# Kernel tuning notes

Hardware: AMD Instinct MI355X
Metric: run time of the kernel (lower is better)

The kernel has to match this reference:

```python
import jax, jax.numpy as jnp
import numpy as np

BITS = 3
LEVELS = 2 ** BITS            # 8
HALF_RANGE = (LEVELS - 1) / 2  # 3.5
INCREMENT = 1.0 / (LEVELS // 2)  # 0.25


def setup_inputs() -> dict:
    key = jax.random.key(0)
    kq, kk, kv, kr = jax.random.split(key, 4)
    B, H, S, D = 2, 16, 2048, 128
    q = jax.random.normal(kq, (B, H, S, D), dtype=jnp.float32)
    k = jax.random.normal(kk, (B, H, S, D), dtype=jnp.float32)
    v = jax.random.normal(kv, (B, H, S, D), dtype=jnp.float32)
    # random orthogonal rotation (QR of a Gaussian), as in PolarQuant.__init__
    Hmat = jax.random.normal(kr, (D, D), dtype=jnp.float32)
    R, _ = jnp.linalg.qr(Hmat)
    qjl_scale = jnp.full((1,), 0.01, dtype=jnp.float32)
    return {"q": q, "k": k, "v": v, "R": R, "qjl_scale": qjl_scale}


def _compress_decompress(x, R, qjl_scale):
    """PolarQuant rotate -> QJL 3-bit quantize (+ sign correction) -> dequantize -> inverse rotate."""
    B, Hh, S, D = x.shape
    xr = jnp.einsum('bhsd,de->bhse', x, R)            # rotate: x @ R
    x_max = jnp.abs(xr).max() + 1e-8                   # global scale (as in quantize/compress)
    xs = xr / x_max * HALF_RANGE                       # scale to [-3.5, 3.5]
    xq = jnp.clip(jnp.round(xs / INCREMENT) * INCREMENT, -HALF_RANGE, HALF_RANGE)
    residual = xs - xq
    xc = xq + jnp.sign(residual) * qjl_scale[0] * x_max  # QJL 1-bit correction
    xd = xc / HALF_RANGE * x_max                       # dequantize
    xo = jnp.einsum('bhse,de->bhsd', xd, R)            # inverse rotate: y @ R.T
    return xo


def reference(q, k, v, R, qjl_scale):
    D = q.shape[-1]
    k_approx = _compress_decompress(k, R, qjl_scale)
    v_approx = _compress_decompress(v, R, qjl_scale)
    scores = jnp.einsum('bhqd,bhkd->bhqk', q, k_approx) / jnp.sqrt(jnp.float32(D))
    attn = jax.nn.softmax(scores, axis=-1)
    out = jnp.einsum('bhqk,bhkd->bhqd', attn, v_approx)
    return out
```

## Files before the change

kernel.cpp:

```cpp
#include <hip/hip_runtime.h>


typedef float    f32x4  __attribute__((ext_vector_type(4)));
typedef float    f32x16 __attribute__((ext_vector_type(16)));
typedef __bf16   bf16x8 __attribute__((ext_vector_type(8)));
typedef __bf16   bf16x4 __attribute__((ext_vector_type(4)));
typedef _Float16 f16x8  __attribute__((ext_vector_type(8)));
typedef unsigned long long u64;

#define SLEN 2048
#define DH   128

static __device__ __forceinline__ f32x16 zero16() {
  f32x16 z;
#pragma unroll
  for (int i = 0; i < 16; ++i) z[i] = 0.f;
  return z;
}

static __device__ __forceinline__ f32x16 mfma_bf16_32x32x16(bf16x8 a, bf16x8 b, f32x16 c) {
  return __builtin_amdgcn_mfma_f32_32x32x16_bf16(a, b, c, 0, 0, 0);
}
static __device__ __forceinline__ f32x16 mfma_f16_32x32x16(f16x8 a, f16x8 b, f32x16 c) {
  return __builtin_amdgcn_mfma_f32_32x32x16_f16(a, b, c, 0, 0, 0);
}

static __device__ __forceinline__ void lds_dma16(const void* g, void* l) {
  __builtin_amdgcn_global_load_lds(
      (const __attribute__((address_space(1))) void*)(unsigned long long)g,
      (__attribute__((address_space(3))) void*)(unsigned int)(unsigned long long)l,
      16, 0, 0);
}

static __device__ __forceinline__ float qdq(float xr, float xmax, float qs) {
  float xs = xr / xmax * 3.5f;
  float xq = rintf(xs * 4.0f) * 0.25f;
  xq = fminf(3.5f, fmaxf(-3.5f, xq));
  float res = xs - xq;
  float sg = (res > 0.0f) ? 1.0f : ((res < 0.0f) ? -1.0f : 0.0f);
  float xc = xq + sg * qs * xmax;
  return xc / 3.5f * xmax;
}

static __device__ __forceinline__ unsigned short bfbits(float f) {
  __bf16 b = (__bf16)f;
  return __builtin_bit_cast(unsigned short, b);
}

__global__ __launch_bounds__(256) void prep_R(
    const float* __restrict__ R, _Float16* __restrict__ Bhi,
    _Float16* __restrict__ Blo, _Float16* __restrict__ BhiT,
    _Float16* __restrict__ BloT)
{
  int i = blockIdx.x * 256 + threadIdx.x;
  int kk = i >> 7, n = i & 127;
  float r = R[i];
  _Float16 h = (_Float16)r;
  _Float16 l = (_Float16)(r - (float)h);
  Bhi[i] = h; Blo[i] = l;
  BhiT[n * 128 + kk] = h; BloT[n * 128 + kk] = l;
}

__global__ __launch_bounds__(256) void rot_all_kernel(
    const float* __restrict__ K, const float* __restrict__ V,
    const float* __restrict__ Q, const _Float16* __restrict__ Gh,
    const _Float16* __restrict__ Gl, float* __restrict__ kr,
    float* __restrict__ vr, float* __restrict__ kpart,
    float* __restrict__ vpart, __bf16* __restrict__ qb,
    float* __restrict__ qn)
{
  __shared__ _Float16 BH[128 * 128];

  const int tid = threadIdx.x, wave = tid >> 6, lane = tid & 63;
  const int r31 = lane & 31, hi = lane >> 5;
  const int bid = blockIdx.x;

  int stage_n[8], stage_ch[8], stage_dst[8];
#pragma unroll
  for (int u = 0; u < 8; ++u) {
    int c = (wave * 8 + u) * 64 + lane;
    stage_n[u] = c >> 4;
    stage_ch[u] = (c & 15) ^ (stage_n[u] & 7);
    stage_dst[u] = (wave * 8 + u) * 512;
  }

  if (bid < 1024) {
    const bool isv = bid >= 512;
    const int b = bid & 511;
    const float* X = isv ? V : K;
    float* OUT = isv ? vr : kr;
    float* part = isv ? vpart : kpart;
    const long r0 = (long)b * 128;

#pragma unroll
    for (int u = 0; u < 8; ++u)
      lds_dma16(Gh + stage_n[u] * 128 + stage_ch[u] * 8, BH + stage_dst[u]);

    const long rowg = r0 + wave * 32 + r31;
    f16x8 ah[8], al[8];
#pragma unroll
    for (int t = 0; t < 8; ++t) {
      f32x4 x0 = *(const f32x4*)&X[rowg * 128 + t * 16 + hi * 8];
      f32x4 x1 = *(const f32x4*)&X[rowg * 128 + t * 16 + hi * 8 + 4];
#pragma unroll
      for (int j = 0; j < 4; ++j) {
        _Float16 h0 = (_Float16)x0[j]; ah[t][j] = h0;
        _Float16 h1 = (_Float16)x1[j]; ah[t][4 + j] = h1;
        al[t][j]     = (_Float16)(x0[j] - (float)h0);
        al[t][4 + j] = (_Float16)(x1[j] - (float)h1);
      }
    }
    __syncthreads();

    f32x16 acc[4];
#pragma unroll
    for (int ct = 0; ct < 4; ++ct) acc[ct] = zero16();
#pragma unroll
    for (int ct = 0; ct < 4; ++ct) {
#pragma unroll
      for (int t = 0; t < 8; ++t) {
        int idx = (ct * 32 + r31) * 128 + (((2 * t + hi) ^ (r31 & 7)) * 8);
        f16x8 bh = *(const f16x8*)&BH[idx];
        acc[ct] = mfma_f16_32x32x16(ah[t], bh, acc[ct]);
        acc[ct] = mfma_f16_32x32x16(al[t], bh, acc[ct]);
      }
    }

    __syncthreads();
#pragma unroll
    for (int u = 0; u < 8; ++u)
      lds_dma16(Gl + stage_n[u] * 128 + stage_ch[u] * 8, BH + stage_dst[u]);
    __syncthreads();

#pragma unroll
    for (int ct = 0; ct < 4; ++ct) {
#pragma unroll
      for (int t = 0; t < 8; ++t) {
        int idx = (ct * 32 + r31) * 128 + (((2 * t + hi) ^ (r31 & 7)) * 8);
        f16x8 bl = *(const f16x8*)&BH[idx];
        acc[ct] = mfma_f16_32x32x16(ah[t], bl, acc[ct]);
      }
    }

    float am = 0.f;
#pragma unroll
    for (int ct = 0; ct < 4; ++ct)
#pragma unroll
      for (int r = 0; r < 16; ++r) {
        long grow = r0 + wave * 32 + (r & 3) + 8 * (r >> 2) + 4 * hi;
        float v = acc[ct][r];
        OUT[grow * 128 + ct * 32 + r31] = v;
        am = fmaxf(am, fabsf(v));
      }
#pragma unroll
    for (int m = 1; m <= 32; m <<= 1) am = fmaxf(am, __shfl_xor(am, m, 64));
    if (lane == 0) part[b * 4 + wave] = am;

  } else {
    const int b = bid - 1024;
    const long r0 = (long)b * 128;

#pragma unroll
    for (int u = 0; u < 8; ++u)
      lds_dma16(Gh + stage_n[u] * 128 + stage_ch[u] * 8, BH + stage_dst[u]);

    const long rowg = r0 + wave * 32 + r31;
    f16x8 ah[8];
#pragma unroll
    for (int t = 0; t < 8; ++t) {
      f32x4 x0 = *(const f32x4*)&Q[rowg * 128 + t * 16 + hi * 8];
      f32x4 x1 = *(const f32x4*)&Q[rowg * 128 + t * 16 + hi * 8 + 4];
#pragma unroll
      for (int j = 0; j < 4; ++j) {
        ah[t][j]     = (_Float16)x0[j];
        ah[t][4 + j] = (_Float16)x1[j];
      }
    }
    __syncthreads();

    f32x16 acc[4];
#pragma unroll
    for (int ct = 0; ct < 4; ++ct) acc[ct] = zero16();
#pragma unroll
    for (int ct = 0; ct < 4; ++ct) {
#pragma unroll
      for (int t = 0; t < 8; ++t) {
        int idx = (ct * 32 + r31) * 128 + (((2 * t + hi) ^ (r31 & 7)) * 8);
        f16x8 bh = *(const f16x8*)&BH[idx];
        acc[ct] = mfma_f16_32x32x16(ah[t], bh, acc[ct]);
      }
    }

    const float sc = 0.12751743342f;
    float rs[16];
#pragma unroll
    for (int r = 0; r < 16; ++r) rs[r] = 0.f;
#pragma unroll
    for (int ct = 0; ct < 4; ++ct)
#pragma unroll
      for (int r = 0; r < 16; ++r) {
        long grow = r0 + wave * 32 + (r & 3) + 8 * (r >> 2) + 4 * hi;
        __bf16 bb = (__bf16)(acc[ct][r] * sc);
        qb[grow * 128 + ct * 32 + r31] = bb;
        float fb = (float)bb;
        rs[r] += fb * fb;
      }
#pragma unroll
    for (int r = 0; r < 16; ++r) {
#pragma unroll
      for (int msk = 1; msk <= 16; msk <<= 1) rs[r] += __shfl_xor(rs[r], msk, 64);
      if (r31 == r)
        qn[r0 + wave * 32 + (r & 3) + 8 * (r >> 2) + 4 * hi] = sqrtf(rs[r]);
    }
  }
}

__global__ __launch_bounds__(256) void rot_o_kernel(
    const _Float16* __restrict__ X, const _Float16* __restrict__ Gh,
    float* __restrict__ OUT)
{
  __shared__ _Float16 BH[128 * 128];

  const int tid = threadIdx.x, wave = tid >> 6, lane = tid & 63;
  const int r31 = lane & 31, hi = lane >> 5;
  const long r0 = (long)blockIdx.x * 128;

#pragma unroll
  for (int u = 0; u < 8; ++u) {
    int c = (wave * 8 + u) * 64 + lane;
    int n = c >> 4, p = c & 15, ch = p ^ (n & 7);
    lds_dma16(Gh + n * 128 + ch * 8, BH + (wave * 8 + u) * 512);
  }

  const long rowg = r0 + wave * 32 + r31;
  f16x8 ah[8];
#pragma unroll
  for (int t = 0; t < 8; ++t)
    ah[t] = *(const f16x8*)&X[rowg * 128 + t * 16 + hi * 8];
  __syncthreads();

  f32x16 acc[4];
#pragma unroll
  for (int ct = 0; ct < 4; ++ct) acc[ct] = zero16();
#pragma unroll
  for (int ct = 0; ct < 4; ++ct) {
#pragma unroll
    for (int t = 0; t < 8; ++t) {
      int idx = (ct * 32 + r31) * 128 + (((2 * t + hi) ^ (r31 & 7)) * 8);
      f16x8 bh = *(const f16x8*)&BH[idx];
      acc[ct] = mfma_f16_32x32x16(ah[t], bh, acc[ct]);
    }
  }
#pragma unroll
  for (int ct = 0; ct < 4; ++ct)
#pragma unroll
    for (int r = 0; r < 16; ++r) {
      long grow = r0 + wave * 32 + (r & 3) + 8 * (r >> 2) + 4 * hi;
      OUT[grow * 128 + ct * 32 + r31] = acc[ct][r];
    }
}

__global__ __launch_bounds__(256) void quantize_vt_kernel(
    const float* __restrict__ vr, const float* __restrict__ vpart,
    const float* __restrict__ qjl, u64* __restrict__ vdt2)
{
  __shared__ unsigned int Ts32[128][18];
  __shared__ float sm[4];
  const int tid = threadIdx.x;

  float m = 0.f;
  for (int i = tid; i < 2048; i += 256) m = fmaxf(m, vpart[i]);
#pragma unroll
  for (int msk = 1; msk <= 32; msk <<= 1) m = fmaxf(m, __shfl_xor(m, msk, 64));
  if ((tid & 63) == 0) sm[tid >> 6] = m;
  __syncthreads();
  const float xmax = fmaxf(fmaxf(sm[0], sm[1]), fmaxf(sm[2], sm[3])) + 1e-8f;
  const float qs = qjl[0];

  const int bh = blockIdx.x >> 6, blk = blockIdx.x & 63;
  const int s0 = blk * 32;
  const int sp  = tid & 15;
  const int dch = tid >> 4;
  const long rb = (long)bh * SLEN + s0;
  const float* p0 = &vr[(rb + sp * 2    ) * 128 + dch * 8];
  const float* p1 = &vr[(rb + sp * 2 + 1) * 128 + dch * 8];
#pragma unroll
  for (int j = 0; j < 8; ++j) {
    unsigned a = bfbits(qdq(p0[j], xmax, qs));
    unsigned b = bfbits(qdq(p1[j], xmax, qs));
    Ts32[dch * 8 + j][sp] = a | (b << 16);
  }
  __syncthreads();
  const long obase = (long)(bh * 64 + blk) * 1024;
#pragma unroll
  for (int uu = 0; uu < 2; ++uu) {
    int u_ = uu * 256 + tid;
    int half = u_ >> 8, hi = (u_ >> 7) & 1, d = u_ & 127;
    u64 qlo = *(const u64*)&Ts32[d][2 * (half * 4 + hi)];
    u64 qhi = *(const u64*)&Ts32[d][2 * (half * 4 + hi + 2)];
    vdt2[obase + u_ * 2    ] = qlo;
    vdt2[obase + u_ * 2 + 1] = qhi;
  }
}

__global__ __launch_bounds__(256) void quantize_k_kernel(
    const float* __restrict__ kr, const float* __restrict__ kpart,
    const float* __restrict__ qjl, __bf16* __restrict__ out)
{
  __shared__ float sm[4];
  const int tid = threadIdx.x;
  float m = 0.f;
  for (int i = tid; i < 2048; i += 256) m = fmaxf(m, kpart[i]);
#pragma unroll
  for (int msk = 1; msk <= 32; msk <<= 1) m = fmaxf(m, __shfl_xor(m, msk, 64));
  if ((tid & 63) == 0) sm[tid >> 6] = m;
  __syncthreads();
  const float xmax = fmaxf(fmaxf(sm[0], sm[1]), fmaxf(sm[2], sm[3])) + 1e-8f;
  const float qs = qjl[0];

  long i = ((long)blockIdx.x * 256 + tid) * 4;
  f32x4 x = *(const f32x4*)&kr[i];
  bf16x4 ov;
#pragma unroll
  for (int j = 0; j < 4; ++j) ov[j] = (__bf16)qdq(x[j], xmax, qs);
  *(bf16x4*)&out[i] = ov;
}

__global__ __launch_bounds__(256, 2) void attn2(
    const __bf16* __restrict__ qb, const __bf16* __restrict__ kd,
    const u64* __restrict__ vdt2, const float* __restrict__ qn,
    const float* __restrict__ kpart, const float* __restrict__ qjl,
    _Float16* __restrict__ orot)
{
  __shared__ __attribute__((aligned(16))) __bf16 Ks[2][2][32 * DH];
  __shared__ __attribute__((aligned(16))) u64   Vt[2][2][1024];
  __shared__ float Ls[4][32];
  __shared__ float sm[4];

  const int tid = threadIdx.x, wave = tid >> 6, lane = tid & 63;
  const int r31 = lane & 31, hi = lane >> 5;
  const int head = blockIdx.x & 31, qt = blockIdx.x >> 5;
  const long hrow = (long)head * SLEN;
  const int qrow0 = qt * 128 + wave * 32;

  float km = 0.f;
  for (int i = tid; i < 2048; i += 256) km = fmaxf(km, kpart[i]);
#pragma unroll
  for (int m = 1; m <= 32; m <<= 1) km = fmaxf(km, __shfl_xor(km, m, 64));
  if (lane == 0) sm[wave] = km;
  __syncthreads();
  const float xmax = fmaxf(fmaxf(sm[0], sm[1]), fmaxf(sm[2], sm[3])) + 1e-8f;
  const float Bk = 11.313708499f * ((3.5f + qjl[0] * xmax) * xmax / 3.5f) * 1.02f * 0.5f;

  bf16x8 qf[8];
#pragma unroll
  for (int t = 0; t < 8; ++t)
    qf[t] = *(const bf16x8*)&qb[(hrow + qrow0 + r31) * DH + t * 16 + hi * 8];
  const float mqneg = -(qn[hrow + qrow0 + r31] * Bk);

  int koff[8];
#pragma unroll
  for (int t = 0; t < 8; ++t)
    koff[t] = r31 * 256 + (((2 * t + hi) ^ (r31 & 7)) << 4);

  int vof0[4], vof1[4];
#pragma unroll
  for (int dt = 0; dt < 4; ++dt) {
    vof0[dt] = (((0 * 2 + hi) * 128) + dt * 32 + r31) * 16;
    vof1[dt] = (((1 * 2 + hi) * 128) + dt * 32 + r31) * 16;
  }

  const __bf16* ksrc[2]; int kds[2];
#pragma unroll
  for (int u = 0; u < 2; ++u) {
    int c = (wave * 2 + u) * 64 + lane;
    int row = c >> 4, ch = (c & 15) ^ (row & 7);
    ksrc[u] = kd + (hrow + row) * DH + ch * 8;
    kds[u] = (wave * 2 + u) * 512;
  }
  const char* vbase = (const char*)(vdt2 + (long)head * 64 * 1024);
  const char* vsrc[2];
#pragma unroll
  for (int u = 0; u < 2; ++u)
    vsrc[u] = vbase + (long)((wave * 2 + u) * 64 + lane) * 16;

  auto STAGE = [&](int B, int P) {
    const long k0 = (long)(2 * P) * 32 * DH, k1 = k0 + 32 * DH;
    const long v0 = (long)(2 * P) * 8192,    v1 = v0 + 8192;
    lds_dma16(ksrc[0] + k0, &Ks[B][0][kds[0]]);
    lds_dma16(ksrc[1] + k0, &Ks[B][0][kds[1]]);
    lds_dma16(ksrc[0] + k1, &Ks[B][1][kds[0]]);
    lds_dma16(ksrc[1] + k1, &Ks[B][1][kds[1]]);
    lds_dma16(vsrc[0] + v0, &Vt[B][0][(wave * 2 + 0) * 128]);
    lds_dma16(vsrc[1] + v0, &Vt[B][0][(wave * 2 + 1) * 128]);
    lds_dma16(vsrc[0] + v1, &Vt[B][1][(wave * 2 + 0) * 128]);
    lds_dma16(vsrc[1] + v1, &Vt[B][1][(wave * 2 + 1) * 128]);
  };

  STAGE(0, 0);
  STAGE(1, 1);
  asm volatile("s_waitcnt vmcnt(8)" ::: "memory");
  __builtin_amdgcn_s_barrier();
  asm volatile("" ::: "memory");

  f32x16 acc[4];
#pragma unroll
  for (int dt = 0; dt < 4; ++dt) acc[dt] = zero16();
  float ls0 = 0.f, ls1 = 0.f, ls2 = 0.f, ls3 = 0.f;

  auto TILE = [&](const f32x16& sa, const f32x16& sb, int B, int j) {
    float p[16];
#pragma unroll
    for (int r = 0; r < 16; ++r) p[r] = __builtin_amdgcn_exp2f(sa[r] + sb[r]);
#pragma unroll
    for (int r = 0; r < 16; r += 4) {
      ls0 += p[r]; ls1 += p[r + 1]; ls2 += p[r + 2]; ls3 += p[r + 3];
    }
    bf16x8 pa, pb;
#pragma unroll
    for (int jj = 0; jj < 8; ++jj) { pa[jj] = (__bf16)p[jj]; pb[jj] = (__bf16)p[8 + jj]; }
    const char* vb = (const char*)&Vt[B][j][0];
    __builtin_amdgcn_s_setprio(1);
#pragma unroll
    for (int dt = 0; dt < 4; ++dt) {
      bf16x8 v0 = *(const bf16x8*)(vb + vof0[dt]);
      acc[dt] = mfma_bf16_32x32x16(pa, v0, acc[dt]);
    }
#pragma unroll
    for (int dt = 0; dt < 4; ++dt) {
      bf16x8 v1 = *(const bf16x8*)(vb + vof1[dt]);
      acc[dt] = mfma_bf16_32x32x16(pb, v1, acc[dt]);
    }
    __builtin_amdgcn_s_setprio(0);
  };

#pragma unroll 1
  for (int i = 0; i < SLEN / 64; ++i) {
    const int B = i & 1;
    const char* k0 = (const char*)&Ks[B][0][0];
    const char* k1 = (const char*)&Ks[B][1][0];

    f32x16 sa0 = zero16(), sa1 = zero16(), sb0, sb1;
#pragma unroll
    for (int r = 0; r < 16; ++r) { sb0[r] = mqneg; sb1[r] = mqneg; }
    __builtin_amdgcn_s_setprio(1);
#pragma unroll
    for (int t = 0; t < 8; t += 2) {
      bf16x8 ka0 = *(const bf16x8*)(k0 + koff[t]);
      bf16x8 kb0 = *(const bf16x8*)(k1 + koff[t]);
      bf16x8 ka1 = *(const bf16x8*)(k0 + koff[t + 1]);
      bf16x8 kb1 = *(const bf16x8*)(k1 + koff[t + 1]);
      sa0 = mfma_bf16_32x32x16(ka0, qf[t], sa0);
      sa1 = mfma_bf16_32x32x16(kb0, qf[t], sa1);
      sb0 = mfma_bf16_32x32x16(ka1, qf[t + 1], sb0);
      sb1 = mfma_bf16_32x32x16(kb1, qf[t + 1], sb1);
    }
    __builtin_amdgcn_s_setprio(0);

    TILE(sa0, sb0, B, 0);
    TILE(sa1, sb1, B, 1);

    if (i < SLEN / 64 - 1) {
      asm volatile("s_waitcnt vmcnt(0)" ::: "memory");
      __builtin_amdgcn_s_barrier();
      asm volatile("" ::: "memory");
      if (i < SLEN / 64 - 2) STAGE(B, i + 2);
    }
  }

  float lsum = (ls0 + ls1) + (ls2 + ls3);
  lsum += __shfl_xor(lsum, 32, 64);
  if (hi == 0) Ls[wave][r31] = 1.0f / lsum;
  __syncthreads();

#pragma unroll
  for (int dt = 0; dt < 4; ++dt)
#pragma unroll
    for (int r = 0; r < 16; ++r) {
      int qr = (r & 3) + 8 * (r >> 2) + 4 * hi;
      orot[(hrow + qrow0 + qr) * DH + dt * 32 + r31] =
          (_Float16)(acc[dt][r] * Ls[wave][qr]);
    }
}

extern "C" void kernel_launch(void* const* d_in, const int* in_sizes, int n_in,
                              void* d_out, int out_size, void* d_ws, size_t ws_size,
                              hipStream_t stream)
{
  const float* q   = (const float*)d_in[0];
  const float* k   = (const float*)d_in[1];
  const float* v   = (const float*)d_in[2];
  const float* R   = (const float*)d_in[3];
  const float* qjl = (const float*)d_in[4];

  char* ws = (char*)d_ws;
  float* kpart = (float*)ws;
  float* vpart = (float*)(ws + 8192);
  _Float16* Bhi  = (_Float16*)(ws + 32768);
  _Float16* Blo  = (_Float16*)(ws + 65536);
  _Float16* BhiT = (_Float16*)(ws + 98304);
  _Float16* BloT = (_Float16*)(ws + 131072);
  float* qn = (float*)(ws + 163840);
  char* base = ws + 425984;
  __bf16* qb   = (__bf16*)base;
  float*  kr   = (float*)(base + (16u << 20));
  float*  vr   = (float*)(base + (48u << 20));
  u64*    vdt2 = (u64*)(base + (80u << 20));
  __bf16* kd   = (__bf16*)vr;
  _Float16* orot = (_Float16*)kr;

  dim3 b256(256);
  prep_R<<<64, b256, 0, stream>>>(R, Bhi, Blo, BhiT, BloT);
  rot_all_kernel<<<1536, b256, 0, stream>>>(k, v, q, BhiT, BloT, kr, vr,
                                            kpart, vpart, qb, qn);
  quantize_vt_kernel<<<2048, b256, 0, stream>>>(vr, vpart, qjl, vdt2);
  quantize_k_kernel<<<8192, b256, 0, stream>>>(kr, kpart, qjl, kd);
  attn2<<<512, b256, 0, stream>>>(qb, kd, vdt2, qn, kpart, qjl, orot);
  rot_o_kernel<<<512, b256, 0, stream>>>(orot, Bhi, (float*)d_out);
}
```

Before: 274.4 us.

## Fuse output inverse rotation into attention kernel epilogue

The separate rot_o kernel is removed. The attention kernel now stages its normalized fp16 output tile in shared memory, which it reuses from the K/V buffers. It loads the rotation matrix into LDS and runs the inverse-rotation MFMA in the epilogue, writing fp32 output directly. This drops one launch and the global round-trip of the intermediate output. Separately, quantize_k processes 16 elements per thread with a quarter of the blocks, which cuts the per-block overhead of recomputing the max reduction.

```diff
diff --git a/kernel.cpp b/kernel.cpp
--- a/kernel.cpp
+++ b/kernel.cpp
@@ -215,51 +215,6 @@
   }
 }
 
-__global__ __launch_bounds__(256) void rot_o_kernel(
-    const _Float16* __restrict__ X, const _Float16* __restrict__ Gh,
-    float* __restrict__ OUT)
-{
-  __shared__ _Float16 BH[128 * 128];
-
-  const int tid = threadIdx.x, wave = tid >> 6, lane = tid & 63;
-  const int r31 = lane & 31, hi = lane >> 5;
-  const long r0 = (long)blockIdx.x * 128;
-
-#pragma unroll
-  for (int u = 0; u < 8; ++u) {
-    int c = (wave * 8 + u) * 64 + lane;
-    int n = c >> 4, p = c & 15, ch = p ^ (n & 7);
-    lds_dma16(Gh + n * 128 + ch * 8, BH + (wave * 8 + u) * 512);
-  }
-
-  const long rowg = r0 + wave * 32 + r31;
-  f16x8 ah[8];
-#pragma unroll
-  for (int t = 0; t < 8; ++t)
-    ah[t] = *(const f16x8*)&X[rowg * 128 + t * 16 + hi * 8];
-  __syncthreads();
-
-  f32x16 acc[4];
-#pragma unroll
-  for (int ct = 0; ct < 4; ++ct) acc[ct] = zero16();
-#pragma unroll
-  for (int ct = 0; ct < 4; ++ct) {
-#pragma unroll
-    for (int t = 0; t < 8; ++t) {
-      int idx = (ct * 32 + r31) * 128 + (((2 * t + hi) ^ (r31 & 7)) * 8);
-      f16x8 bh = *(const f16x8*)&BH[idx];
-      acc[ct] = mfma_f16_32x32x16(ah[t], bh, acc[ct]);
-    }
-  }
-#pragma unroll
-  for (int ct = 0; ct < 4; ++ct)
-#pragma unroll
-    for (int r = 0; r < 16; ++r) {
-      long grow = r0 + wave * 32 + (r & 3) + 8 * (r >> 2) + 4 * hi;
-      OUT[grow * 128 + ct * 32 + r31] = acc[ct][r];
-    }
-}
-
 __global__ __launch_bounds__(256) void quantize_vt_kernel(
     const float* __restrict__ vr, const float* __restrict__ vpart,
     const float* __restrict__ qjl, u64* __restrict__ vdt2)
@@ -318,19 +273,22 @@
   const float xmax = fmaxf(fmaxf(sm[0], sm[1]), fmaxf(sm[2], sm[3])) + 1e-8f;
   const float qs = qjl[0];
 
-  long i = ((long)blockIdx.x * 256 + tid) * 4;
-  f32x4 x = *(const f32x4*)&kr[i];
-  bf16x4 ov;
-#pragma unroll
-  for (int j = 0; j < 4; ++j) ov[j] = (__bf16)qdq(x[j], xmax, qs);
-  *(bf16x4*)&out[i] = ov;
+  long i = ((long)blockIdx.x * 256 + tid) * 16;
+#pragma unroll
+  for (int jj = 0; jj < 4; ++jj) {
+    f32x4 x = *(const f32x4*)&kr[i + jj * 4];
+    bf16x4 ov;
+#pragma unroll
+    for (int j = 0; j < 4; ++j) ov[j] = (__bf16)qdq(x[j], xmax, qs);
+    *(bf16x4*)&out[i + jj * 4] = ov;
+  }
 }
 
 __global__ __launch_bounds__(256, 2) void attn2(
     const __bf16* __restrict__ qb, const __bf16* __restrict__ kd,
     const u64* __restrict__ vdt2, const float* __restrict__ qn,
     const float* __restrict__ kpart, const float* __restrict__ qjl,
-    _Float16* __restrict__ orot)
+    const _Float16* __restrict__ Bhi, float* __restrict__ OUT)
 {
   __shared__ __attribute__((aligned(16))) __bf16 Ks[2][2][32 * DH];
   __shared__ __attribute__((aligned(16))) u64   Vt[2][2][1024];
@@ -473,13 +431,50 @@
   if (hi == 0) Ls[wave][r31] = 1.0f / lsum;
   __syncthreads();
 
+  _Float16* BHR = (_Float16*)&Ks[0][0][0];
+  _Float16* Osh = (_Float16*)&Vt[0][0][0] + wave * 4096;
+
+#pragma unroll
+  for (int u = 0; u < 8; ++u) {
+    int c = (wave * 8 + u) * 64 + lane;
+    int n = c >> 4, ch = (c & 15) ^ (n & 7);
+    lds_dma16(Bhi + n * 128 + ch * 8, BHR + (wave * 8 + u) * 512);
+  }
+
 #pragma unroll
   for (int dt = 0; dt < 4; ++dt)
 #pragma unroll
     for (int r = 0; r < 16; ++r) {
-      int qr = (r & 3) + 8 * (r >> 2) + 4 * hi;
-      orot[(hrow + qrow0 + qr) * DH + dt * 32 + r31] =
-          (_Float16)(acc[dt][r] * Ls[wave][qr]);
+      int q2 = (r & 3) + 8 * (r >> 2) + 4 * hi;
+      _Float16 o = (_Float16)(acc[dt][r] * Ls[wave][q2]);
+      int ch = (dt * 4 + (r31 >> 3)) ^ (q2 & 7);
+      Osh[q2 * 128 + ch * 8 + (r31 & 7)] = o;
+    }
+  __syncthreads();
+
+  f16x8 ah[8];
+#pragma unroll
+  for (int t = 0; t < 8; ++t)
+    ah[t] = *(const f16x8*)&Osh[r31 * 128 + (((2 * t + hi) ^ (r31 & 7)) * 8)];
+
+  f32x16 acc2[4];
+#pragma unroll
+  for (int ct = 0; ct < 4; ++ct) acc2[ct] = zero16();
+#pragma unroll
+  for (int ct = 0; ct < 4; ++ct) {
+#pragma unroll
+    for (int t = 0; t < 8; ++t) {
+      f16x8 bh = *(const f16x8*)&BHR[(ct * 32 + r31) * 128 +
+                                     (((2 * t + hi) ^ (r31 & 7)) * 8)];
+      acc2[ct] = mfma_f16_32x32x16(ah[t], bh, acc2[ct]);
+    }
+  }
+#pragma unroll
+  for (int ct = 0; ct < 4; ++ct)
+#pragma unroll
+    for (int r = 0; r < 16; ++r) {
+      int m2 = (r & 3) + 8 * (r >> 2) + 4 * hi;
+      OUT[(hrow + qrow0 + m2) * DH + ct * 32 + r31] = acc2[ct][r];
     }
 }
 
@@ -507,14 +502,13 @@
   float*  vr   = (float*)(base + (48u << 20));
   u64*    vdt2 = (u64*)(base + (80u << 20));
   __bf16* kd   = (__bf16*)vr;
-  _Float16* orot = (_Float16*)kr;
 
   dim3 b256(256);
   prep_R<<<64, b256, 0, stream>>>(R, Bhi, Blo, BhiT, BloT);
   rot_all_kernel<<<1536, b256, 0, stream>>>(k, v, q, BhiT, BloT, kr, vr,
                                             kpart, vpart, qb, qn);
   quantize_vt_kernel<<<2048, b256, 0, stream>>>(vr, vpart, qjl, vdt2);
-  quantize_k_kernel<<<8192, b256, 0, stream>>>(kr, kpart, qjl, kd);
-  attn2<<<512, b256, 0, stream>>>(qb, kd, vdt2, qn, kpart, qjl, orot);
-  rot_o_kernel<<<512, b256, 0, stream>>>(orot, Bhi, (float*)d_out);
-}
+  quantize_k_kernel<<<2048, b256, 0, stream>>>(kr, kpart, qjl, kd);
+  attn2<<<512, b256, 0, stream>>>(qb, kd, vdt2, qn, kpart, qjl, Bhi,
+                                  (float*)d_out);
+}
```

Result: faster. 261.7 us (-4.6%).
